# Performance work log

Hardware: AMD Instinct MI355X
Metric: run time of the kernel (lower is better)

## Reference

```python
import jax, jax.numpy as jnp
import numpy as np

N, D, K = 65536, 1024, 256

def setup_inputs() -> dict:
    key = jax.random.key(0)
    k1, k2 = jax.random.split(key)
    inputs = jax.random.normal(k1, (N, D), dtype=jnp.float32)
    centroids = jax.random.normal(k2, (K, D), dtype=jnp.float32)
    return {"inputs": inputs, "centroids": centroids}

def reference(inputs, centroids):
    # Squared euclidean distances [K, N] without materializing [K, N, D]:
    # ||c||^2 + ||x||^2 - 2 c @ x^T  (same math as sum(square(x[None]-c[:,None]), -1))
    x_sq = jnp.sum(inputs * inputs, axis=1)            # [N]
    c_sq = jnp.sum(centroids * centroids, axis=1)      # [K]
    cross = jnp.einsum('kd,nd->kn', centroids, inputs) # [K, N]
    distances = c_sq[:, None] + x_sq[None, :] - 2.0 * cross  # [K, N]
    assignments = jnp.argmin(distances, axis=0)        # [N], int
    # calculate_loss: sum_c mean(where(assign==c, distances, 0)) over the full
    # [K,N] grid. Since each n matches exactly one cluster c, the per-cluster
    # masked means sum to the global mean of distances.
    loss = jnp.mean(distances)
    return distances, assignments, loss
```

## Files before the change

### kernel.cpp

```cpp
#include <hip/hip_runtime.h>
#include <cstdint>

#define N_PTS 65536
#define DIM   1024
#define K_CL  256
#define BN    256
#define BK    32
#define NT    (DIM / BK)
#define THREADS 512

typedef __bf16 bf16_t;
typedef bf16_t bf16x8 __attribute__((ext_vector_type(8)));
typedef float  f32x4  __attribute__((ext_vector_type(4)));

union U16x8 { uint4 u4; bf16x8 bf; ushort us[8]; };

__device__ __forceinline__ ushort f2bf_rne(float f) {
    uint32_t u = __float_as_uint(f);
    uint32_t r = (u + 0x7FFFu + ((u >> 16) & 1u)) >> 16;
    return (ushort)r;
}
__device__ __forceinline__ float bf2f(ushort b) {
    return __uint_as_float(((uint32_t)b) << 16);
}

__device__ __forceinline__ void gll16(const void* g, void* l) {
    __builtin_amdgcn_global_load_lds(
        (const __attribute__((address_space(1))) void*)g,
        (__attribute__((address_space(3))) void*)l, 16, 0, 0);
}

#define BAR()   __builtin_amdgcn_s_barrier()
#define LGKM0() do { asm volatile("s_waitcnt lgkmcnt(0)" ::: "memory"); \
                     __builtin_amdgcn_sched_barrier(0); } while (0)
#define VMCNT(N) do { asm volatile("s_waitcnt vmcnt(" #N ")" ::: "memory"); \
                      __builtin_amdgcn_sched_barrier(0); } while (0)

__global__ __launch_bounds__(128) void km_prep(const float* __restrict__ cent,
                                               ushort* __restrict__ Ahi,
                                               ushort* __restrict__ Alo,
                                               float* __restrict__ csq) {
    const int r  = blockIdx.x;
    const int j  = threadIdx.x;
    const int kt = j >> 2;
    const int gp = j & 3;
    const int s  = (r >> 1) & 3;
    const int d0 = kt * BK + ((gp ^ s) << 3);

    const float* src = cent + r * DIM + d0;
    float4 a = *(const float4*)src;
    float4 b = *(const float4*)(src + 4);
    float v[8] = {a.x, a.y, a.z, a.w, b.x, b.y, b.z, b.w};

    U16x8 hi, lo;
    float ss = 0.f;
#pragma unroll
    for (int i = 0; i < 8; ++i) {
        float f = v[i];
        ss += f * f;
        ushort h = f2bf_rne(f);
        hi.us[i] = h;
        lo.us[i] = f2bf_rne(f - bf2f(h));
    }
    *(uint4*)(Ahi + kt * (K_CL * BK) + r * BK + gp * 8) = hi.u4;
    *(uint4*)(Alo + kt * (K_CL * BK) + r * BK + gp * 8) = lo.u4;

#pragma unroll
    for (int off = 1; off < 64; off <<= 1) ss += __shfl_xor(ss, off);
    __shared__ float ws2[2];
    if ((j & 63) == 0) ws2[j >> 6] = ss;
    __syncthreads();
    if (j == 0) csq[r] = ws2[0] + ws2[1];
}

__global__ __launch_bounds__(THREADS, 2) void km_main(
    const float* __restrict__ x,
    const ushort* __restrict__ Ahi, const ushort* __restrict__ Alo,
    const float* __restrict__ csq,
    float* __restrict__ out_dist, float* __restrict__ out_assign,
    float* __restrict__ partials) {

    __shared__ __align__(16) ushort sAhi[2][K_CL * BK];
    __shared__ __align__(16) ushort sAlo[2][K_CL * BK];
    __shared__ __align__(16) ushort sBhi[2][BN * BK];
    __shared__ __align__(16) ushort sBlo[2][BN * BK];
    __shared__ __align__(16) float  sCsq[K_CL];
    __shared__ __align__(16) float  sXsq[BN];
    __shared__ float sRedV[4 * BN];
    __shared__ int   sRedI[4 * BN];
    __shared__ float sWsum[8];

    const int tid  = threadIdx.x;
    const int blk  = blockIdx.x;
    const int lane = tid & 63;
    const int w    = tid >> 6;
    const int wr   = w >> 1;
    const int wc   = w & 1;
    const int l15  = lane & 15;
    const int l4   = lane >> 4;

    if (tid < K_CL) sCsq[tid] = csq[tid];

    const int bcol  = tid >> 1;
    const int bhalf = tid & 1;
    const int bs    = (bcol >> 1) & 3;
    const int bOff0 = bcol * BK + ((((bhalf << 1) | 0) ^ bs) << 3);
    const int bOff1 = bcol * BK + ((((bhalf << 1) | 1) ^ bs) << 3);
    const float* xsrc = x + (size_t)(blk * BN + bcol) * DIM + bhalf * 16;

    float xs_acc = 0.f;

    auto stageA_hi = [&](int kt, int buf) {
        const char* ph = (const char*)Ahi + kt * 16384 + tid * 16;
        char* dh = (char*)&sAhi[buf][0] + tid * 16;
        gll16(ph, dh);
        gll16(ph + 8192, dh + 8192);
    };
    auto stageA_lo = [&](int kt, int buf) {
        const char* pl = (const char*)Alo + kt * 16384 + tid * 16;
        char* dl = (char*)&sAlo[buf][0] + tid * 16;
        gll16(pl, dl);
        gll16(pl + 8192, dl + 8192);
    };
    auto writeB = [&](int buf, float4 v0, float4 v1, float4 v2, float4 v3) {
        float f[16] = {v0.x, v0.y, v0.z, v0.w, v1.x, v1.y, v1.z, v1.w,
                       v2.x, v2.y, v2.z, v2.w, v3.x, v3.y, v3.z, v3.w};
        U16x8 h0, h1, l0, l1;
#pragma unroll
        for (int i = 0; i < 8; ++i) {
            float a = f[i];
            xs_acc = fmaf(a, a, xs_acc);
            bf16_t hb = (bf16_t)a;
            h0.bf[i] = hb;
            l0.bf[i] = (bf16_t)(a - (float)hb);
            float b = f[i + 8];
            xs_acc = fmaf(b, b, xs_acc);
            bf16_t hc = (bf16_t)b;
            h1.bf[i] = hc;
            l1.bf[i] = (bf16_t)(b - (float)hc);
        }
        *(uint4*)&sBhi[buf][bOff0] = h0.u4;
        *(uint4*)&sBhi[buf][bOff1] = h1.u4;
        *(uint4*)&sBlo[buf][bOff0] = l0.u4;
        *(uint4*)&sBlo[buf][bOff1] = l1.u4;
    };

    int aOff[4], bOff[8];
#pragma unroll
    for (int f = 0; f < 4; ++f) {
        int row  = wr * 64 + f * 16 + l15;
        aOff[f]  = row * BK + ((l4 ^ ((row >> 1) & 3)) << 3);
    }
#pragma unroll
    for (int f = 0; f < 8; ++f) {
        int col  = wc * 128 + f * 16 + l15;
        bOff[f]  = col * BK + ((l4 ^ ((col >> 1) & 3)) << 3);
    }

    float4 b0, b1, b2, b3;
    stageA_hi(0, 0);
    stageA_lo(0, 0);
    b0 = *(const float4*)(xsrc);
    b1 = *(const float4*)(xsrc + 4);
    b2 = *(const float4*)(xsrc + 8);
    b3 = *(const float4*)(xsrc + 12);
    writeB(0, b0, b1, b2, b3);
    __syncthreads();

    f32x4 acc[4][8];
#pragma unroll
    for (int i = 0; i < 4; ++i)
#pragma unroll
        for (int q = 0; q < 8; ++q) acc[i][q] = (f32x4){0.f, 0.f, 0.f, 0.f};

#define MFMA_PAIR(FJ)                                                                                  \
    _Pragma("unroll")                                                                                  \
    for (int fi = 0; fi < 4; ++fi) {                                                                   \
        acc[fi][FJ]     = __builtin_amdgcn_mfma_f32_16x16x32_bf16(ah[fi].bf, bhx.bf, acc[fi][FJ], 0, 0, 0);     \
        acc[fi][FJ]     = __builtin_amdgcn_mfma_f32_16x16x32_bf16(ah[fi].bf, blx.bf, acc[fi][FJ], 0, 0, 0);     \
        acc[fi][FJ]     = __builtin_amdgcn_mfma_f32_16x16x32_bf16(al[fi].bf, bhx.bf, acc[fi][FJ], 0, 0, 0);     \
        acc[fi][FJ + 1] = __builtin_amdgcn_mfma_f32_16x16x32_bf16(ah[fi].bf, bhy.bf, acc[fi][FJ + 1], 0, 0, 0); \
        acc[fi][FJ + 1] = __builtin_amdgcn_mfma_f32_16x16x32_bf16(ah[fi].bf, bly.bf, acc[fi][FJ + 1], 0, 0, 0); \
        acc[fi][FJ + 1] = __builtin_amdgcn_mfma_f32_16x16x32_bf16(al[fi].bf, bhy.bf, acc[fi][FJ + 1], 0, 0, 0); \
    }

#define DS_READ_PAIR(FJ)                                  \
    bhx.u4 = *(const uint4*)&sBhi[cur][bOff[FJ]];         \
    blx.u4 = *(const uint4*)&sBlo[cur][bOff[FJ]];         \
    bhy.u4 = *(const uint4*)&sBhi[cur][bOff[(FJ) + 1]];   \
    bly.u4 = *(const uint4*)&sBlo[cur][bOff[(FJ) + 1]];

    for (int kt = 0; kt < NT; ++kt) {
        const int  cur = kt & 1, nxt = cur ^ 1;
        const bool pf  = (kt + 1 < NT);

        U16x8 ah[4], al[4], bhx, blx, bhy, bly;

        if (pf) {
            const float* p = xsrc + (kt + 1) * BK;
            b0 = *(const float4*)p;
            b1 = *(const float4*)(p + 4);
            b2 = *(const float4*)(p + 8);
            b3 = *(const float4*)(p + 12);
        }
#pragma unroll
        for (int f = 0; f < 4; ++f) {
            ah[f].u4 = *(const uint4*)&sAhi[cur][aOff[f]];
            al[f].u4 = *(const uint4*)&sAlo[cur][aOff[f]];
        }
        DS_READ_PAIR(0)
        if (pf) stageA_hi(kt + 1, nxt);
        __builtin_amdgcn_sched_barrier(0);
        BAR();
        LGKM0();
        __builtin_amdgcn_s_setprio(1);
        MFMA_PAIR(0)
        __builtin_amdgcn_s_setprio(0);
        BAR();

        DS_READ_PAIR(2)
        if (pf) stageA_lo(kt + 1, nxt);
        __builtin_amdgcn_sched_barrier(0);
        BAR();
        LGKM0();
        __builtin_amdgcn_s_setprio(1);
        MFMA_PAIR(2)
        __builtin_amdgcn_s_setprio(0);
        BAR();

        DS_READ_PAIR(4)
        __builtin_amdgcn_sched_barrier(0);
        BAR();
        LGKM0();
        __builtin_amdgcn_s_setprio(1);
        MFMA_PAIR(4)
        __builtin_amdgcn_s_setprio(0);
        BAR();

        DS_READ_PAIR(6)
        if (pf) {
            VMCNT(4);
            writeB(nxt, b0, b1, b2, b3);
        }
        __builtin_amdgcn_sched_barrier(0);
        BAR();
        LGKM0();
        __builtin_amdgcn_s_setprio(1);
        MFMA_PAIR(6)
        __builtin_amdgcn_s_setprio(0);
        if (pf) VMCNT(0);
        BAR();
    }
#undef MFMA_PAIR
#undef DS_READ_PAIR

    {
        float v = xs_acc;
        v += __shfl_xor(v, 1);
        if (bhalf == 0) sXsq[bcol] = v;
    }
    __syncthreads();

    const int colBase = wc * 128;
    float xs[8];
    f32x4 cs[4];
#pragma unroll
    for (int f = 0; f < 8; ++f) xs[f] = sXsq[colBase + f * 16 + l15];
#pragma unroll
    for (int f = 0; f < 4; ++f) cs[f] = *(const f32x4*)&sCsq[wr * 64 + f * 16 + l4 * 4];

    float lsum = 0.f;
    float bestv[8];
    int   bestr[8];
#pragma unroll
    for (int f = 0; f < 8; ++f) { bestv[f] = 3.4e38f; bestr[f] = 0; }

#pragma unroll
    for (int fi = 0; fi < 4; ++fi) {
        const int rowB = wr * 64 + fi * 16 + l4 * 4;
#pragma unroll
        for (int fj = 0; fj < 8; ++fj) {
            const int col = blk * BN + colBase + fj * 16 + l15;
            float* outp = out_dist + (size_t)rowB * N_PTS + col;
#pragma unroll
            for (int j = 0; j < 4; ++j) {
                float d = cs[fi][j] + xs[fj] - 2.0f * acc[fi][fj][j];
                outp[(size_t)j * N_PTS] = d;
                lsum += d;
                int r = rowB + j;
                if (d < bestv[fj]) { bestv[fj] = d; bestr[fj] = r; }
            }
        }
    }

#pragma unroll
    for (int fj = 0; fj < 8; ++fj) {
#pragma unroll
        for (int m = 16; m <= 32; m <<= 1) {
            float ov = __shfl_xor(bestv[fj], m);
            int   orr = __shfl_xor(bestr[fj], m);
            if (ov < bestv[fj] || (ov == bestv[fj] && orr < bestr[fj])) {
                bestv[fj] = ov; bestr[fj] = orr;
            }
        }
        if (lane < 16) {
            sRedV[wr * BN + colBase + fj * 16 + lane] = bestv[fj];
            sRedI[wr * BN + colBase + fj * 16 + lane] = bestr[fj];
        }
    }

#pragma unroll
    for (int off = 1; off < 64; off <<= 1) lsum += __shfl_xor(lsum, off);
    if (lane == 0) sWsum[w] = lsum;
    __syncthreads();

    if (tid < BN) {
        float bv = sRedV[tid];
        int   br = sRedI[tid];
#pragma unroll
        for (int q = 1; q < 4; ++q) {
            float v = sRedV[q * BN + tid];
            int   r = sRedI[q * BN + tid];
            if (v < bv || (v == bv && r < br)) { bv = v; br = r; }
        }
        out_assign[blk * BN + tid] = (float)br;
    }
    if (tid == 0) {
        float t = 0.f;
#pragma unroll
        for (int q = 0; q < 8; ++q) t += sWsum[q];
        partials[blk] = t;
    }
}

__global__ __launch_bounds__(256) void km_fin(const float* __restrict__ partials,
                                              float* __restrict__ out_loss) {
    __shared__ float ws[4];
    const int t = threadIdx.x;
    float v = partials[t];
#pragma unroll
    for (int off = 1; off < 64; off <<= 1) v += __shfl_xor(v, off);
    if ((t & 63) == 0) ws[t >> 6] = v;
    __syncthreads();
    if (t == 0) {
        float s = 0.f;
#pragma unroll
        for (int i = 0; i < 4; ++i) s += ws[i];
        out_loss[0] = s / 16777216.0f;
    }
}

extern "C" void kernel_launch(void* const* d_in, const int* in_sizes, int n_in,
                              void* d_out, int out_size, void* d_ws, size_t ws_size,
                              hipStream_t stream) {
    const float* x    = (const float*)d_in[0];
    const float* cent = (const float*)d_in[1];

    float* out        = (float*)d_out;
    float* out_dist   = out;
    float* out_assign = out + (size_t)K_CL * N_PTS;
    float* out_loss   = out_assign + N_PTS;

    char*   ws       = (char*)d_ws;
    float*  csq      = (float*)ws;
    float*  partials = (float*)(ws + 1024);
    ushort* Ahi      = (ushort*)(ws + 4096);
    ushort* Alo      = (ushort*)(ws + 4096 + 524288);

    km_prep<<<dim3(K_CL), dim3(128), 0, stream>>>(cent, Ahi, Alo, csq);
    km_main<<<dim3(N_PTS / BN), dim3(THREADS), 0, stream>>>(
        x, Ahi, Alo, csq, out_dist, out_assign, partials);
    km_fin<<<dim3(1), dim3(256), 0, stream>>>(partials, out_loss);
}
```

Baseline: 121.8 us.

## Reorder split-bf16 MFMA phases and split B-tile conversion across phases

Restructures the per-k-tile schedule of the three-term split-bf16 GEMM. The first three phases now issue the hi*hi and hi*lo products with the MFMAs grouped by B fragment. The final phase does all lo*hi products, so the A-lo fragments are read later and B fragments stay in registers across phases. The fp32-to-bf16 hi/lo conversion and LDS write of the next B tile is split into two halves placed in different phases, spreading VALU work and hiding load waits. This holds all 8 B hi/lo fragments live at once, raising register pressure, and the VMCNT counts must match the outstanding loads.

```diff
diff --git a/kernel.cpp b/kernel.cpp
--- a/kernel.cpp
+++ b/kernel.cpp
@@ -31,10 +31,12 @@
 }
 
 #define BAR()   __builtin_amdgcn_s_barrier()
+#define SCHB()  __builtin_amdgcn_sched_barrier(0)
 #define LGKM0() do { asm volatile("s_waitcnt lgkmcnt(0)" ::: "memory"); \
                      __builtin_amdgcn_sched_barrier(0); } while (0)
 #define VMCNT(N) do { asm volatile("s_waitcnt vmcnt(" #N ")" ::: "memory"); \
                       __builtin_amdgcn_sched_barrier(0); } while (0)
+#define MFMA(ACC, A, B) (ACC) = __builtin_amdgcn_mfma_f32_16x16x32_bf16((A).bf, (B).bf, (ACC), 0, 0, 0)
 
 __global__ __launch_bounds__(128) void km_prep(const float* __restrict__ cent,
                                                ushort* __restrict__ Ahi,
@@ -122,27 +124,20 @@
         gll16(pl, dl);
         gll16(pl + 8192, dl + 8192);
     };
-    auto writeB = [&](int buf, float4 v0, float4 v1, float4 v2, float4 v3) {
-        float f[16] = {v0.x, v0.y, v0.z, v0.w, v1.x, v1.y, v1.z, v1.w,
-                       v2.x, v2.y, v2.z, v2.w, v3.x, v3.y, v3.z, v3.w};
-        U16x8 h0, h1, l0, l1;
+    auto writeB_half = [&](int buf, float4 u, float4 v, int half) {
+        float f[8] = {u.x, u.y, u.z, u.w, v.x, v.y, v.z, v.w};
+        U16x8 h, l;
 #pragma unroll
         for (int i = 0; i < 8; ++i) {
             float a = f[i];
             xs_acc = fmaf(a, a, xs_acc);
             bf16_t hb = (bf16_t)a;
-            h0.bf[i] = hb;
-            l0.bf[i] = (bf16_t)(a - (float)hb);
-            float b = f[i + 8];
-            xs_acc = fmaf(b, b, xs_acc);
-            bf16_t hc = (bf16_t)b;
-            h1.bf[i] = hc;
-            l1.bf[i] = (bf16_t)(b - (float)hc);
-        }
-        *(uint4*)&sBhi[buf][bOff0] = h0.u4;
-        *(uint4*)&sBhi[buf][bOff1] = h1.u4;
-        *(uint4*)&sBlo[buf][bOff0] = l0.u4;
-        *(uint4*)&sBlo[buf][bOff1] = l1.u4;
+            h.bf[i] = hb;
+            l.bf[i] = (bf16_t)(a - (float)hb);
+        }
+        const int off = half ? bOff1 : bOff0;
+        *(uint4*)&sBhi[buf][off] = h.u4;
+        *(uint4*)&sBlo[buf][off] = l.u4;
     };
 
     int aOff[4], bOff[8];
@@ -164,7 +159,8 @@
     b1 = *(const float4*)(xsrc + 4);
     b2 = *(const float4*)(xsrc + 8);
     b3 = *(const float4*)(xsrc + 12);
-    writeB(0, b0, b1, b2, b3);
+    writeB_half(0, b0, b1, 0);
+    writeB_half(0, b2, b3, 1);
     __syncthreads();
 
     f32x4 acc[4][8];
@@ -172,29 +168,12 @@
     for (int i = 0; i < 4; ++i)
 #pragma unroll
         for (int q = 0; q < 8; ++q) acc[i][q] = (f32x4){0.f, 0.f, 0.f, 0.f};
-
-#define MFMA_PAIR(FJ)                                                                                  \
-    _Pragma("unroll")                                                                                  \
-    for (int fi = 0; fi < 4; ++fi) {                                                                   \
-        acc[fi][FJ]     = __builtin_amdgcn_mfma_f32_16x16x32_bf16(ah[fi].bf, bhx.bf, acc[fi][FJ], 0, 0, 0);     \
-        acc[fi][FJ]     = __builtin_amdgcn_mfma_f32_16x16x32_bf16(ah[fi].bf, blx.bf, acc[fi][FJ], 0, 0, 0);     \
-        acc[fi][FJ]     = __builtin_amdgcn_mfma_f32_16x16x32_bf16(al[fi].bf, bhx.bf, acc[fi][FJ], 0, 0, 0);     \
-        acc[fi][FJ + 1] = __builtin_amdgcn_mfma_f32_16x16x32_bf16(ah[fi].bf, bhy.bf, acc[fi][FJ + 1], 0, 0, 0); \
-        acc[fi][FJ + 1] = __builtin_amdgcn_mfma_f32_16x16x32_bf16(ah[fi].bf, bly.bf, acc[fi][FJ + 1], 0, 0, 0); \
-        acc[fi][FJ + 1] = __builtin_amdgcn_mfma_f32_16x16x32_bf16(al[fi].bf, bhy.bf, acc[fi][FJ + 1], 0, 0, 0); \
-    }
-
-#define DS_READ_PAIR(FJ)                                  \
-    bhx.u4 = *(const uint4*)&sBhi[cur][bOff[FJ]];         \
-    blx.u4 = *(const uint4*)&sBlo[cur][bOff[FJ]];         \
-    bhy.u4 = *(const uint4*)&sBhi[cur][bOff[(FJ) + 1]];   \
-    bly.u4 = *(const uint4*)&sBlo[cur][bOff[(FJ) + 1]];
 
     for (int kt = 0; kt < NT; ++kt) {
         const int  cur = kt & 1, nxt = cur ^ 1;
         const bool pf  = (kt + 1 < NT);
 
-        U16x8 ah[4], al[4], bhx, blx, bhy, bly;
+        U16x8 ah[4], al[4], bh[8], bl[8];
 
         if (pf) {
             const float* p = xsrc + (kt + 1) * BK;
@@ -204,55 +183,89 @@
             b3 = *(const float4*)(p + 12);
         }
 #pragma unroll
-        for (int f = 0; f < 4; ++f) {
-            ah[f].u4 = *(const uint4*)&sAhi[cur][aOff[f]];
-            al[f].u4 = *(const uint4*)&sAlo[cur][aOff[f]];
-        }
-        DS_READ_PAIR(0)
+        for (int f = 0; f < 4; ++f) ah[f].u4 = *(const uint4*)&sAhi[cur][aOff[f]];
+        bh[0].u4 = *(const uint4*)&sBhi[cur][bOff[0]];
+        bh[1].u4 = *(const uint4*)&sBhi[cur][bOff[1]];
+        bl[0].u4 = *(const uint4*)&sBlo[cur][bOff[0]];
+        bl[1].u4 = *(const uint4*)&sBlo[cur][bOff[1]];
         if (pf) stageA_hi(kt + 1, nxt);
-        __builtin_amdgcn_sched_barrier(0);
+        SCHB();
         BAR();
         LGKM0();
         __builtin_amdgcn_s_setprio(1);
-        MFMA_PAIR(0)
+#pragma unroll
+        for (int fj = 0; fj < 2; ++fj)
+#pragma unroll
+            for (int fi = 0; fi < 4; ++fi) MFMA(acc[fi][fj], ah[fi], bh[fj]);
+#pragma unroll
+        for (int fj = 0; fj < 2; ++fj)
+#pragma unroll
+            for (int fi = 0; fi < 4; ++fi) MFMA(acc[fi][fj], ah[fi], bl[fj]);
         __builtin_amdgcn_s_setprio(0);
         BAR();
 
-        DS_READ_PAIR(2)
+#pragma unroll
+        for (int f = 0; f < 4; ++f) al[f].u4 = *(const uint4*)&sAlo[cur][aOff[f]];
+        bh[2].u4 = *(const uint4*)&sBhi[cur][bOff[2]];
+        bh[3].u4 = *(const uint4*)&sBhi[cur][bOff[3]];
+        bl[2].u4 = *(const uint4*)&sBlo[cur][bOff[2]];
+        bl[3].u4 = *(const uint4*)&sBlo[cur][bOff[3]];
         if (pf) stageA_lo(kt + 1, nxt);
-        __builtin_amdgcn_sched_barrier(0);
+        SCHB();
         BAR();
         LGKM0();
         __builtin_amdgcn_s_setprio(1);
-        MFMA_PAIR(2)
+#pragma unroll
+        for (int fj = 2; fj < 4; ++fj)
+#pragma unroll
+            for (int fi = 0; fi < 4; ++fi) MFMA(acc[fi][fj], ah[fi], bh[fj]);
+#pragma unroll
+        for (int fj = 2; fj < 4; ++fj)
+#pragma unroll
+            for (int fi = 0; fi < 4; ++fi) MFMA(acc[fi][fj], ah[fi], bl[fj]);
         __builtin_amdgcn_s_setprio(0);
         BAR();
 
-        DS_READ_PAIR(4)
-        __builtin_amdgcn_sched_barrier(0);
+#pragma unroll
+        for (int f = 4; f < 8; ++f) {
+            bh[f].u4 = *(const uint4*)&sBhi[cur][bOff[f]];
+            bl[f].u4 = *(const uint4*)&sBlo[cur][bOff[f]];
+        }
+        if (pf) {
+            VMCNT(6);
+            writeB_half(nxt, b0, b1, 0);
+        }
+        SCHB();
         BAR();
         LGKM0();
         __builtin_amdgcn_s_setprio(1);
-        MFMA_PAIR(4)
+#pragma unroll
+        for (int fj = 4; fj < 8; ++fj)
+#pragma unroll
+            for (int fi = 0; fi < 4; ++fi) MFMA(acc[fi][fj], ah[fi], bh[fj]);
+#pragma unroll
+        for (int fj = 4; fj < 8; ++fj)
+#pragma unroll
+            for (int fi = 0; fi < 4; ++fi) MFMA(acc[fi][fj], ah[fi], bl[fj]);
         __builtin_amdgcn_s_setprio(0);
         BAR();
 
-        DS_READ_PAIR(6)
         if (pf) {
             VMCNT(4);
-            writeB(nxt, b0, b1, b2, b3);
-        }
-        __builtin_amdgcn_sched_barrier(0);
+            writeB_half(nxt, b2, b3, 1);
+        }
+        SCHB();
         BAR();
         LGKM0();
         __builtin_amdgcn_s_setprio(1);
-        MFMA_PAIR(6)
+#pragma unroll
+        for (int fj = 0; fj < 8; ++fj)
+#pragma unroll
+            for (int fi = 0; fi < 4; ++fi) MFMA(acc[fi][fj], al[fi], bh[fj]);
         __builtin_amdgcn_s_setprio(0);
         if (pf) VMCNT(0);
         BAR();
     }
-#undef MFMA_PAIR
-#undef DS_READ_PAIR
 
     {
         float v = xs_acc;
```

Result: slower. 128.6 us (+5.5%).
